# Kernel tuning notes

Hardware: AMD Instinct MI355X
Metric: run time of the kernel (lower is better)

Reference implementation:

```python
import jax, jax.numpy as jnp
import numpy as np

BASE_MARGIN = 0.1
N = 8192


def setup_inputs() -> dict:
    key = jax.random.key(0)
    k1, k2, k3 = jax.random.split(key, 3)
    predictions = jax.random.normal(k1, (N,), dtype=jnp.float32)
    targets = jax.random.normal(k2, (N,), dtype=jnp.float32)
    uncertainties = jax.random.uniform(k3, (N,), dtype=jnp.float32)
    return {"predictions": predictions, "targets": targets, "uncertainties": uncertainties}


def reference(predictions, targets, uncertainties):
    n = predictions.shape[0]
    # pairwise differences, [n, n]; entry (i, j) corresponds to pair (i, j)
    tdiff = targets[:, None] - targets[None, :]
    pdiff = predictions[:, None] - predictions[None, :]
    # adaptive margin: base_margin * clamp(|t_i - t_j|, 0.1, 1.0)
    margin = BASE_MARGIN * jnp.clip(jnp.abs(tdiff), 0.1, 1.0)
    # uncertainty weight: 1 / (1 + u_i + u_j)
    weight = 1.0 / (1.0 + uncertainties[:, None] + uncertainties[None, :])
    # if t_i > t_j: hinge(p_j - p_i + margin) = hinge(-pdiff + margin)
    # if t_j > t_i: hinge(p_i - p_j + margin) = hinge(+pdiff + margin)
    sgn = jnp.sign(tdiff)
    hinge = jnp.maximum(-sgn * pdiff + margin, 0.0)
    # only upper-triangular pairs (i < j) with t_i != t_j contribute
    iu = jnp.triu(jnp.ones((n, n), dtype=bool), k=1)
    mask = iu & (tdiff != 0.0)
    loss = jnp.sum(jnp.where(mask, weight * hinge, 0.0))
    count = jnp.sum(mask)
    return loss / jnp.maximum(count, 1).astype(loss.dtype)
```

## Files before the change

### kernel.cpp

```cpp
#include <hip/hip_runtime.h>


constexpr int TILE = 128;

__device__ __forceinline__ void pair_op(float pi, float ti, float ui1,
                                        const float4& v, bool extra_ok,
                                        float& acc, float& cntf)
{
    const float tdiff = ti - v.x;
    const float pdiff = pi - v.y;
    const float m3 = __builtin_amdgcn_fmed3f(fabsf(tdiff), 0.1f, 1.0f);
    const float spd = __uint_as_float(__float_as_uint(pdiff) ^
                                      (__float_as_uint(tdiff) & 0x80000000u));
    const float h = fmaxf(fmaf(m3, 0.1f, -spd), 0.0f);
    const float w = __builtin_amdgcn_rcpf(ui1 + v.z);
    const bool use = (tdiff != 0.0f) && extra_ok;
    acc  = fmaf(use ? w : 0.0f, h, acc);
    cntf += use ? 1.0f : 0.0f;
}

__global__ __launch_bounds__(TILE) void arl_pair_kernel(
    const float* __restrict__ pred, const float* __restrict__ targ,
    const float* __restrict__ unc, int n, int nt,
    float2* __restrict__ partials)
{
    const int k = blockIdx.x;
    int r = (int)((float)nt + 0.5f - sqrtf(((float)nt + 0.5f) * ((float)nt + 0.5f)
                                           - 2.0f * (float)k));
    if (r < 0) r = 0;
    auto base = [nt](int rr) { return rr * nt - (rr * (rr - 1)) / 2; };
    while (base(r + 1) <= k) ++r;
    while (base(r) > k) --r;
    const int c = r + (k - base(r));

    const int tid = threadIdx.x;
    const int i   = r * TILE + tid;
    const int j0  = c * TILE;

    __shared__ float4 sj[TILE];
    {
        const int jg = j0 + tid;
        const bool v = jg < n;
        sj[tid] = make_float4(v ? targ[jg] : 0.0f, v ? pred[jg] : 0.0f,
                              v ? unc[jg] : 0.0f, 0.0f);
    }
    __syncthreads();

    float acc = 0.0f, cntf = 0.0f;
    const bool full = (j0 + TILE <= n) && (r * TILE + TILE <= n);

    if (i < n) {
        const float pi  = pred[i];
        const float ti  = targ[i];
        const float ui1 = 1.0f + unc[i];
        if (full) {
            if (r != c) {
                #pragma unroll 8
                for (int jj = 0; jj < TILE; ++jj)
                    pair_op(pi, ti, ui1, sj[jj], true, acc, cntf);
            } else {
                #pragma unroll 8
                for (int jj = 0; jj < TILE; ++jj)
                    pair_op(pi, ti, ui1, sj[jj], (j0 + jj) > i, acc, cntf);
            }
        } else {
            const int jmax = (n - j0 < TILE) ? (n - j0) : TILE;
            for (int jj = 0; jj < jmax; ++jj)
                pair_op(pi, ti, ui1, sj[jj], (j0 + jj) > i, acc, cntf);
        }
    }

    for (int off = 32; off > 0; off >>= 1) {
        acc  += __shfl_down(acc, off);
        cntf += __shfl_down(cntf, off);
    }
    __shared__ float sa[TILE / 64], sc[TILE / 64];
    const int lane = tid & 63, wid = tid >> 6;
    if (lane == 0) { sa[wid] = acc; sc[wid] = cntf; }
    __syncthreads();
    if (tid == 0) {
        float a2 = 0.0f, c2 = 0.0f;
        #pragma unroll
        for (int w = 0; w < TILE / 64; ++w) { a2 += sa[w]; c2 += sc[w]; }
        partials[k] = float2{a2, c2};
    }
}

__global__ __launch_bounds__(256) void arl_finalize(
    const float2* __restrict__ partials, int nPartials, float* __restrict__ out)
{
    float a = 0.0f, c = 0.0f;
    for (int k = threadIdx.x; k < nPartials; k += 256) {
        const float2 v = partials[k];
        a += v.x; c += v.y;
    }
    for (int off = 32; off > 0; off >>= 1) {
        a += __shfl_down(a, off);
        c += __shfl_down(c, off);
    }
    __shared__ float sa[4], sc[4];
    const int lane = threadIdx.x & 63, wid = threadIdx.x >> 6;
    if (lane == 0) { sa[wid] = a; sc[wid] = c; }
    __syncthreads();
    if (threadIdx.x == 0) {
        double A = 0.0, C = 0.0;
        #pragma unroll
        for (int w = 0; w < 4; ++w) { A += (double)sa[w]; C += (double)sc[w]; }
        out[0] = (float)(A / (C > 0.0 ? C : 1.0));
    }
}

extern "C" void kernel_launch(void* const* d_in, const int* in_sizes, int n_in,
                              void* d_out, int out_size, void* d_ws, size_t ws_size,
                              hipStream_t stream) {
    const float* pred = (const float*)d_in[0];
    const float* targ = (const float*)d_in[1];
    const float* unc  = (const float*)d_in[2];
    const int n = in_sizes[0];

    const int nt = (n + TILE - 1) / TILE;
    const int nTiles = nt * (nt + 1) / 2;
    float2* partials = (float2*)d_ws;

    arl_pair_kernel<<<nTiles, TILE, 0, stream>>>(pred, targ, unc, n, nt, partials);
    arl_finalize<<<1, 256, 0, stream>>>(partials, nTiles, (float*)d_out);
}
```

Measured before the change: 75.81 us.

## Switch to per-wave 64x64 tiles with register broadcast and ballot counting

Each wavefront now handles its own 64x64 triangular tile, with four independent tiles per block. The j-values are held in registers and broadcast with readlane instead of being staged through shared memory, which removes the LDS round-trip and the block barrier. The pair count is now taken with ballot and popcount into a scalar integer instead of a per-lane float add. The diagonal tiles are finer, so less work is wasted on masked pairs, but there are more tiles, more partials and more triangular index math per tile.

```diff
diff --git a/kernel.cpp b/kernel.cpp
--- a/kernel.cpp
+++ b/kernel.cpp
@@ -1,88 +1,100 @@
 #include <hip/hip_runtime.h>
 
 
-constexpr int TILE = 128;
+constexpr int CH  = 64;
+constexpr int WPB = 4;
 
-__device__ __forceinline__ void pair_op(float pi, float ti, float ui1,
-                                        const float4& v, bool extra_ok,
-                                        float& acc, float& cntf)
-{
-    const float tdiff = ti - v.x;
-    const float pdiff = pi - v.y;
-    const float m3 = __builtin_amdgcn_fmed3f(fabsf(tdiff), 0.1f, 1.0f);
-    const float spd = __uint_as_float(__float_as_uint(pdiff) ^
-                                      (__float_as_uint(tdiff) & 0x80000000u));
-    const float h = fmaxf(fmaf(m3, 0.1f, -spd), 0.0f);
-    const float w = __builtin_amdgcn_rcpf(ui1 + v.z);
-    const bool use = (tdiff != 0.0f) && extra_ok;
-    acc  = fmaf(use ? w : 0.0f, h, acc);
-    cntf += use ? 1.0f : 0.0f;
+__device__ __forceinline__ float bcastf(float v, int lane) {
+    return __int_as_float(__builtin_amdgcn_readlane(__float_as_int(v), lane));
 }
 
-__global__ __launch_bounds__(TILE) void arl_pair_kernel(
+template<bool DIAG, bool EDGE>
+__device__ __forceinline__ void chunk64(
+    float pi, float ti, float ui1, bool ivalid,
+    float tjv, float pjv, float ujv,
+    int i, int j0, int n,
+    float& acc, unsigned& cnt)
+{
+    #pragma unroll
+    for (int jj = 0; jj < CH; ++jj) {
+        const float tj = bcastf(tjv, jj);
+        const float pj = bcastf(pjv, jj);
+        const float uj = bcastf(ujv, jj);
+        const float tdiff = ti - tj;
+        const float pdiff = pi - pj;
+        const float m3 = __builtin_amdgcn_fmed3f(fabsf(tdiff), 0.1f, 1.0f);
+        const float spd = __uint_as_float(__float_as_uint(pdiff) ^
+                                          (__float_as_uint(tdiff) & 0x80000000u));
+        const float h = fmaxf(fmaf(m3, 0.1f, -spd), 0.0f);
+        const float w = __builtin_amdgcn_rcpf(ui1 + uj);
+        bool use = (tdiff != 0.0f);
+        if (DIAG) use = use && ((j0 + jj) > i);
+        if (EDGE) use = use && ivalid && ((j0 + jj) < n);
+        acc = fmaf(use ? w : 0.0f, h, acc);
+        cnt += (unsigned)__popcll(__ballot(use));
+    }
+}
+
+__global__ __launch_bounds__(CH * WPB) void arl_pair_kernel(
     const float* __restrict__ pred, const float* __restrict__ targ,
-    const float* __restrict__ unc, int n, int nt,
+    const float* __restrict__ unc, int n, int nc, int nTiles,
     float2* __restrict__ partials)
 {
-    const int k = blockIdx.x;
-    int r = (int)((float)nt + 0.5f - sqrtf(((float)nt + 0.5f) * ((float)nt + 0.5f)
-                                           - 2.0f * (float)k));
-    if (r < 0) r = 0;
-    auto base = [nt](int rr) { return rr * nt - (rr * (rr - 1)) / 2; };
-    while (base(r + 1) <= k) ++r;
-    while (base(r) > k) --r;
-    const int c = r + (k - base(r));
+    const int tid    = threadIdx.x;
+    const int lane   = tid & 63;
+    const int wid    = tid >> 6;
+    const int tileId = blockIdx.x * WPB + wid;
 
-    const int tid = threadIdx.x;
-    const int i   = r * TILE + tid;
-    const int j0  = c * TILE;
+    float acc = 0.0f;
+    unsigned cnt = 0;
 
-    __shared__ float4 sj[TILE];
-    {
-        const int jg = j0 + tid;
-        const bool v = jg < n;
-        sj[tid] = make_float4(v ? targ[jg] : 0.0f, v ? pred[jg] : 0.0f,
-                              v ? unc[jg] : 0.0f, 0.0f);
-    }
-    __syncthreads();
+    if (tileId < nTiles) {
+        const float nch = (float)nc + 0.5f;
+        int r = (int)(nch - sqrtf(nch * nch - 2.0f * (float)tileId));
+        if (r < 0) r = 0;
+        if (r > nc - 1) r = nc - 1;
+        auto base = [nc](int rr) { return rr * nc - (rr * (rr - 1)) / 2; };
+        while (r + 1 < nc && base(r + 1) <= tileId) ++r;
+        while (r > 0 && base(r) > tileId) --r;
+        const int c = r + (tileId - base(r));
 
-    float acc = 0.0f, cntf = 0.0f;
-    const bool full = (j0 + TILE <= n) && (r * TILE + TILE <= n);
+        const int i0 = r * CH, j0 = c * CH;
+        const int i  = i0 + lane;
+        const int jg = j0 + lane;
+        const bool full = (i0 + CH <= n) && (j0 + CH <= n);
 
-    if (i < n) {
-        const float pi  = pred[i];
-        const float ti  = targ[i];
-        const float ui1 = 1.0f + unc[i];
         if (full) {
-            if (r != c) {
-                #pragma unroll 8
-                for (int jj = 0; jj < TILE; ++jj)
-                    pair_op(pi, ti, ui1, sj[jj], true, acc, cntf);
-            } else {
-                #pragma unroll 8
-                for (int jj = 0; jj < TILE; ++jj)
-                    pair_op(pi, ti, ui1, sj[jj], (j0 + jj) > i, acc, cntf);
-            }
+            const float pi  = pred[i];
+            const float ti  = targ[i];
+            const float ui1 = 1.0f + unc[i];
+            const float tjv = targ[jg];
+            const float pjv = pred[jg];
+            const float ujv = unc[jg];
+            if (r == c) chunk64<true , false>(pi, ti, ui1, true, tjv, pjv, ujv, i, j0, n, acc, cnt);
+            else        chunk64<false, false>(pi, ti, ui1, true, tjv, pjv, ujv, i, j0, n, acc, cnt);
         } else {
-            const int jmax = (n - j0 < TILE) ? (n - j0) : TILE;
-            for (int jj = 0; jj < jmax; ++jj)
-                pair_op(pi, ti, ui1, sj[jj], (j0 + jj) > i, acc, cntf);
+            const bool iv = i < n, jv = jg < n;
+            const float pi  = iv ? pred[i] : 0.0f;
+            const float ti  = iv ? targ[i] : 0.0f;
+            const float ui1 = 1.0f + (iv ? unc[i] : 0.0f);
+            const float tjv = jv ? targ[jg] : 0.0f;
+            const float pjv = jv ? pred[jg] : 0.0f;
+            const float ujv = jv ? unc[jg] : 0.0f;
+            if (r == c) chunk64<true , true >(pi, ti, ui1, iv, tjv, pjv, ujv, i, j0, n, acc, cnt);
+            else        chunk64<false, true >(pi, ti, ui1, iv, tjv, pjv, ujv, i, j0, n, acc, cnt);
         }
     }
 
-    for (int off = 32; off > 0; off >>= 1) {
-        acc  += __shfl_down(acc, off);
-        cntf += __shfl_down(cntf, off);
-    }
-    __shared__ float sa[TILE / 64], sc[TILE / 64];
-    const int lane = tid & 63, wid = tid >> 6;
-    if (lane == 0) { sa[wid] = acc; sc[wid] = cntf; }
+    for (int off = 32; off > 0; off >>= 1) acc += __shfl_down(acc, off);
+
+    __shared__ float sa[WPB], sc[WPB];
+    if (lane == 0) { sa[wid] = acc; sc[wid] = (float)cnt; }
     __syncthreads();
     if (tid == 0) {
         float a2 = 0.0f, c2 = 0.0f;
         #pragma unroll
-        for (int w = 0; w < TILE / 64; ++w) { a2 += sa[w]; c2 += sc[w]; }
-        partials[k] = float2{a2, c2};
+        for (int w = 0; w < WPB; ++w) { a2 += sa[w]; c2 += sc[w]; }
+        partials[blockIdx.x] = float2{a2, c2};
     }
 }
 
@@ -118,10 +130,13 @@
     const float* unc  = (const float*)d_in[2];
     const int n = in_sizes[0];
 
-    const int nt = (n + TILE - 1) / TILE;
-    const int nTiles = nt * (nt + 1) / 2;
+    const int nc     = (n + CH - 1) / CH;
+    const int nTiles = nc * (nc + 1) / 2;
+    const int nBlocks = (nTiles + WPB - 1) / WPB;
+
     float2* partials = (float2*)d_ws;
 
-    arl_pair_kernel<<<nTiles, TILE, 0, stream>>>(pred, targ, unc, n, nt, partials);
-    arl_finalize<<<1, 256, 0, stream>>>(partials, nTiles, (float*)d_out);
+    arl_pair_kernel<<<nBlocks, CH * WPB, 0, stream>>>(pred, targ, unc, n, nc,
+                                                      nTiles, partials);
+    arl_finalize<<<1, 256, 0, stream>>>(partials, nBlocks, (float*)d_out);
 }
```

After: 77.67 us. 2.5% more time.

## Register-block four i-rows per thread over 64-wide j tiles with ballot counts

Applied to the files above, without the earlier changes.

The pair kernel moves from 128x128 triangular tiles to 1024-row i-bands with 64-column j chunks. Each thread holds four i values in registers, so one shared-memory read of a j element serves four pairs. The per-thread float count is replaced by a wave-level ballot popcount. Tiles strictly above the diagonal band take a hot path with no triangular or bounds masks, while diagonal and edge tiles run a masked path. This cuts LDS traffic and per-pair mask overhead, at the cost of more registers, more complex block-index math and a larger grid of smaller j tiles.

```diff
diff --git a/kernel.cpp b/kernel.cpp
--- a/kernel.cpp
+++ b/kernel.cpp
@@ -1,44 +1,36 @@
 #include <hip/hip_runtime.h>
 
 
-constexpr int TILE = 128;
+constexpr int CH    = 64;
+constexpr int IR    = 4;
+constexpr int WPB   = 4;
+constexpr int IBAND = CH * IR * WPB;
+constexpr int JPB   = IBAND / CH;
 
-__device__ __forceinline__ void pair_op(float pi, float ti, float ui1,
-                                        const float4& v, bool extra_ok,
-                                        float& acc, float& cntf)
-{
-    const float tdiff = ti - v.x;
-    const float pdiff = pi - v.y;
-    const float m3 = __builtin_amdgcn_fmed3f(fabsf(tdiff), 0.1f, 1.0f);
-    const float spd = __uint_as_float(__float_as_uint(pdiff) ^
-                                      (__float_as_uint(tdiff) & 0x80000000u));
-    const float h = fmaxf(fmaf(m3, 0.1f, -spd), 0.0f);
-    const float w = __builtin_amdgcn_rcpf(ui1 + v.z);
-    const bool use = (tdiff != 0.0f) && extra_ok;
-    acc  = fmaf(use ? w : 0.0f, h, acc);
-    cntf += use ? 1.0f : 0.0f;
-}
-
-__global__ __launch_bounds__(TILE) void arl_pair_kernel(
+__global__ __launch_bounds__(CH * WPB) void arl_pair_kernel(
     const float* __restrict__ pred, const float* __restrict__ targ,
-    const float* __restrict__ unc, int n, int nt,
+    const float* __restrict__ unc, int n, int ncj, int nbi, int nTiles,
     float2* __restrict__ partials)
 {
-    const int k = blockIdx.x;
-    int r = (int)((float)nt + 0.5f - sqrtf(((float)nt + 0.5f) * ((float)nt + 0.5f)
-                                           - 2.0f * (float)k));
-    if (r < 0) r = 0;
-    auto base = [nt](int rr) { return rr * nt - (rr * (rr - 1)) / 2; };
-    while (base(r + 1) <= k) ++r;
-    while (base(r) > k) --r;
-    const int c = r + (k - base(r));
+    const int tid  = threadIdx.x;
+    const int lane = tid & 63;
+    const int wid  = tid >> 6;
+    const int k    = blockIdx.x;
 
-    const int tid = threadIdx.x;
-    const int i   = r * TILE + tid;
-    const int j0  = c * TILE;
+    const float A = (float)ncj + 8.0f;
+    int ib = (int)((A - sqrtf(fmaxf(A * A - 32.0f * (float)k, 0.0f))) * 0.0625f);
+    if (ib < 0) ib = 0;
+    if (ib > nbi - 1) ib = nbi - 1;
+    auto base = [ncj](int r) { return r * ncj - 8 * r * (r - 1); };
+    while (ib + 1 < nbi && base(ib + 1) <= k) ++ib;
+    while (ib > 0 && base(ib) > k) --ib;
+    const int jt = JPB * ib + (k - base(ib));
 
-    __shared__ float4 sj[TILE];
-    {
+    const int i0 = ib * IBAND;
+    const int j0 = jt * CH;
+
+    __shared__ float4 sj[CH];
+    if (tid < CH) {
         const int jg = j0 + tid;
         const bool v = jg < n;
         sj[tid] = make_float4(v ? targ[jg] : 0.0f, v ? pred[jg] : 0.0f,
@@ -46,43 +38,83 @@
     }
     __syncthreads();
 
-    float acc = 0.0f, cntf = 0.0f;
-    const bool full = (j0 + TILE <= n) && (r * TILE + TILE <= n);
+    float acc[IR] = {0.f, 0.f, 0.f, 0.f};
+    unsigned cnt = 0;
 
-    if (i < n) {
-        const float pi  = pred[i];
-        const float ti  = targ[i];
-        const float ui1 = 1.0f + unc[i];
-        if (full) {
-            if (r != c) {
-                #pragma unroll 8
-                for (int jj = 0; jj < TILE; ++jj)
-                    pair_op(pi, ti, ui1, sj[jj], true, acc, cntf);
-            } else {
-                #pragma unroll 8
-                for (int jj = 0; jj < TILE; ++jj)
-                    pair_op(pi, ti, ui1, sj[jj], (j0 + jj) > i, acc, cntf);
+    const bool hot = (jt >= JPB * ib + JPB) && (i0 + IBAND <= n) && (j0 + CH <= n);
+
+    if (hot) {
+        float pi[IR], ti[IR], ui1[IR];
+        #pragma unroll
+        for (int kk = 0; kk < IR; ++kk) {
+            const int i = i0 + (wid * IR + kk) * CH + lane;
+            pi[kk]  = pred[i];
+            ti[kk]  = targ[i];
+            ui1[kk] = 1.0f + unc[i];
+        }
+        #pragma unroll 8
+        for (int jj = 0; jj < CH; ++jj) {
+            const float4 v = sj[jj];
+            #pragma unroll
+            for (int kk = 0; kk < IR; ++kk) {
+                const float tdiff = ti[kk] - v.x;
+                const float pdiff = pi[kk] - v.y;
+                const float m3 = __builtin_amdgcn_fmed3f(fabsf(tdiff), 0.1f, 1.0f);
+                const float spd = __uint_as_float(__float_as_uint(pdiff) ^
+                                                  (__float_as_uint(tdiff) & 0x80000000u));
+                const float h = fmaxf(fmaf(m3, 0.1f, -spd), 0.0f);
+                const float w = __builtin_amdgcn_rcpf(ui1[kk] + v.z);
+                const bool nz = (tdiff != 0.0f);
+                acc[kk] = fmaf(nz ? w : 0.0f, h, acc[kk]);
+                cnt += (unsigned)__popcll(__ballot(nz));
             }
-        } else {
-            const int jmax = (n - j0 < TILE) ? (n - j0) : TILE;
-            for (int jj = 0; jj < jmax; ++jj)
-                pair_op(pi, ti, ui1, sj[jj], (j0 + jj) > i, acc, cntf);
+        }
+    } else {
+        bool  iv[IR];
+        int   db[IR];
+        float pi[IR], ti[IR], ui1[IR];
+        #pragma unroll
+        for (int kk = 0; kk < IR; ++kk) {
+            const int ibase = i0 + (wid * IR + kk) * CH;
+            const int i = ibase + lane;
+            db[kk] = j0 - ibase;
+            iv[kk] = i < n;
+            pi[kk]  = iv[kk] ? pred[i] : 0.0f;
+            ti[kk]  = iv[kk] ? targ[i] : 0.0f;
+            ui1[kk] = 1.0f + (iv[kk] ? unc[i] : 0.0f);
+        }
+        #pragma unroll 4
+        for (int jj = 0; jj < CH; ++jj) {
+            const float4 v = sj[jj];
+            const bool jok = (j0 + jj) < n;
+            #pragma unroll
+            for (int kk = 0; kk < IR; ++kk) {
+                const float tdiff = ti[kk] - v.x;
+                const float pdiff = pi[kk] - v.y;
+                const float m3 = __builtin_amdgcn_fmed3f(fabsf(tdiff), 0.1f, 1.0f);
+                const float spd = __uint_as_float(__float_as_uint(pdiff) ^
+                                                  (__float_as_uint(tdiff) & 0x80000000u));
+                const float h = fmaxf(fmaf(m3, 0.1f, -spd), 0.0f);
+                const float w = __builtin_amdgcn_rcpf(ui1[kk] + v.z);
+                const bool use = (tdiff != 0.0f) && ((db[kk] + jj) > lane)
+                                 && iv[kk] && jok;
+                acc[kk] = fmaf(use ? w : 0.0f, h, acc[kk]);
+                cnt += (unsigned)__popcll(__ballot(use));
+            }
         }
     }
 
-    for (int off = 32; off > 0; off >>= 1) {
-        acc  += __shfl_down(acc, off);
-        cntf += __shfl_down(cntf, off);
-    }
-    __shared__ float sa[TILE / 64], sc[TILE / 64];
-    const int lane = tid & 63, wid = tid >> 6;
-    if (lane == 0) { sa[wid] = acc; sc[wid] = cntf; }
+    float acct = (acc[0] + acc[1]) + (acc[2] + acc[3]);
+    for (int off = 32; off > 0; off >>= 1) acct += __shfl_down(acct, off);
+
+    __shared__ float sa[WPB], sc[WPB];
+    if (lane == 0) { sa[wid] = acct; sc[wid] = (float)cnt; }
     __syncthreads();
     if (tid == 0) {
         float a2 = 0.0f, c2 = 0.0f;
         #pragma unroll
-        for (int w = 0; w < TILE / 64; ++w) { a2 += sa[w]; c2 += sc[w]; }
-        partials[k] = float2{a2, c2};
+        for (int w = 0; w < WPB; ++w) { a2 += sa[w]; c2 += sc[w]; }
+        partials[blockIdx.x] = float2{a2, c2};
     }
 }
 
@@ -118,10 +150,13 @@
     const float* unc  = (const float*)d_in[2];
     const int n = in_sizes[0];
 
-    const int nt = (n + TILE - 1) / TILE;
-    const int nTiles = nt * (nt + 1) / 2;
+    const int nbi = (n + IBAND - 1) / IBAND;
+    const int ncj = (n + CH - 1) / CH;
+    const int nTiles = nbi * ncj - 8 * nbi * (nbi - 1);
+
     float2* partials = (float2*)d_ws;
 
-    arl_pair_kernel<<<nTiles, TILE, 0, stream>>>(pred, targ, unc, n, nt, partials);
+    arl_pair_kernel<<<nTiles, CH * WPB, 0, stream>>>(pred, targ, unc, n, ncj,
+                                                     nbi, nTiles, partials);
     arl_finalize<<<1, 256, 0, stream>>>(partials, nTiles, (float*)d_out);
 }
```

Result: slower. 82.31 us (+8.6%).
